# Optimization experiments

Measured on AMD Instinct MI355X. Metric: run time of the kernel, lower is better.

## Reference

```python
import jax, jax.numpy as jnp
import numpy as np

D_MODEL = 512; NHEAD = 8; D_FF = 2048
B = 8; C = 64; P = 128
HALF = D_MODEL // 2        # per-branch embed dim (256)
H_HALF = NHEAD // 2        # per-branch heads (4)
HD = HALF // H_HALF        # per-branch head dim (64)
ROPE_BASE = 10000.0
THETA_SCALE = 2.0 * np.pi
LN_EPS = 1e-5; RMS_EPS = 1e-8


def setup_inputs():
    ks = jax.random.split(jax.random.key(0), 16)
    w = lambda k, s: jax.random.normal(k, s, jnp.float32) * 0.02
    return {
        "src": jax.random.normal(ks[0], (B, C, P, D_MODEL), jnp.float32),
        "coords": jax.random.normal(ks[1], (C, 3), jnp.float32),
        "q_attn": w(ks[2], (D_MODEL,)), "rms_attn": jnp.ones((D_MODEL,), jnp.float32),
        "proj_attn_w": w(ks[3], (D_MODEL, D_MODEL)), "proj_attn_b": jnp.zeros((D_MODEL,), jnp.float32),
        "q_ffn": w(ks[4], (D_MODEL,)), "rms_ffn": jnp.ones((D_MODEL,), jnp.float32),
        "proj_ffn_w": w(ks[5], (D_MODEL, D_MODEL)), "proj_ffn_b": jnp.zeros((D_MODEL,), jnp.float32),
        "ln1_w": jnp.ones((D_MODEL,), jnp.float32), "ln1_b": jnp.zeros((D_MODEL,), jnp.float32),
        "ln2_w": jnp.ones((D_MODEL,), jnp.float32), "ln2_b": jnp.zeros((D_MODEL,), jnp.float32),
        "qkv_s_w": w(ks[6], (3 * HALF, HALF)), "qkv_s_b": jnp.zeros((3 * HALF,), jnp.float32),
        "out_s_w": w(ks[7], (HALF, HALF)), "out_s_b": jnp.zeros((HALF,), jnp.float32),
        "qkv_t_w": w(ks[8], (3 * HALF, HALF)), "qkv_t_b": jnp.zeros((3 * HALF,), jnp.float32),
        "out_t_w": w(ks[9], (HALF, HALF)), "out_t_b": jnp.zeros((HALF,), jnp.float32),
        "w1": w(ks[10], (D_FF, D_MODEL)), "b1": jnp.zeros((D_FF,), jnp.float32),
        "w2": w(ks[11], (D_MODEL, D_FF)), "b2": jnp.zeros((D_MODEL,), jnp.float32),
    }


def _rmsnorm(x, w):
    return x / jnp.sqrt(jnp.mean(x * x, axis=-1, keepdims=True) + RMS_EPS) * w


def _layernorm(x, w, b):
    m = jnp.mean(x, axis=-1, keepdims=True)
    v = jnp.mean((x - m) ** 2, axis=-1, keepdims=True)
    return (x - m) / jnp.sqrt(v + LN_EPS) * w + b


def _attn_residual(src, q, norm_w, proj_w, proj_b):
    # sources = [src] stacked on a leading n-axis (n=1) as in AttentionResidual
    V = src[None]                                  # (n, B, C, P, D)
    K = _rmsnorm(V, norm_w)
    logits = jnp.einsum('d,nbcpd->nbcp', q, K)
    wgt = jax.nn.softmax(logits, axis=0)
    out = jnp.einsum('nbcp,nbcpd->bcpd', wgt, V)
    return out @ proj_w.T + proj_b


def _build_freqs(half, dtype):
    idx = jnp.arange(half, dtype=dtype)
    return 1.0 / ROPE_BASE ** (idx / max(half, 1))


def _coord_rope(coords, half):
    # coords: (L, 3); returns cos, sin of shape (1, 1, L, half)
    axis_ids = jnp.arange(half) % 3
    c = coords - jnp.mean(coords, axis=0, keepdims=True)
    r = jnp.linalg.norm(c, axis=-1)
    c = c / jnp.maximum(jnp.max(r), 1e-6)
    freqs = _build_freqs(half, coords.dtype)
    theta = THETA_SCALE * (c[:, axis_ids] * freqs[None, :])   # (L, half)
    return jnp.cos(theta)[None, None], jnp.sin(theta)[None, None]


def _index_rope(L, half, dtype):
    freqs = _build_freqs(half, dtype)
    pos = jnp.arange(L, dtype=dtype)[:, None]
    theta = pos * freqs[None, :]                               # (L, half)
    return jnp.cos(theta)[None, None], jnp.sin(theta)[None, None]


def _apply_rope(q, k, cos, sin):
    half = q.shape[-1] // 2
    q1, q2 = q[..., :half], q[..., half:]
    k1, k2 = k[..., :half], k[..., half:]
    qr = jnp.concatenate([q1 * cos - q2 * sin, q1 * sin + q2 * cos], axis=-1)
    kr = jnp.concatenate([k1 * cos - k2 * sin, k1 * sin + k2 * cos], axis=-1)
    return qr, kr


def _mha(x, w_qkv, b_qkv, w_o, b_o, H, cos, sin):
    Bx, L, E = x.shape
    Hd = E // H
    qkv = x @ w_qkv.T + b_qkv
    q, k, v = jnp.split(qkv, 3, axis=-1)
    q = q.reshape(Bx, L, H, Hd).transpose(0, 2, 1, 3)   # (B, H, L, Hd)
    k = k.reshape(Bx, L, H, Hd).transpose(0, 2, 1, 3)
    v = v.reshape(Bx, L, H, Hd).transpose(0, 2, 1, 3)
    q, k = _apply_rope(q, k, cos, sin)
    scores = jnp.einsum('bhld,bhmd->bhlm', q, k) * (Hd ** -0.5)
    attn = jax.nn.softmax(scores, axis=-1)
    out = jnp.einsum('bhlm,bhmd->bhld', attn, v)
    out = out.transpose(0, 2, 1, 3).reshape(Bx, L, E)
    return out @ w_o.T + b_o


def reference(src, coords, q_attn, rms_attn, proj_attn_w, proj_attn_b,
              q_ffn, rms_ffn, proj_ffn_w, proj_ffn_b,
              ln1_w, ln1_b, ln2_w, ln2_b,
              qkv_s_w, qkv_s_b, out_s_w, out_s_b,
              qkv_t_w, qkv_t_b, out_t_w, out_t_b,
              w1, b1, w2, b2):
    Bx, Cx, Px, D = src.shape
    half = D // 2
    # --- attention block (pre-norm, attention-residual shortcut) ---
    res1 = _attn_residual(src, q_attn, rms_attn, proj_attn_w, proj_attn_b)
    x = _layernorm(src, ln1_w, ln1_b)
    # spatial branch: attention over channels with coordinate RoPE
    xs = x[..., :half].transpose(0, 2, 1, 3).reshape(Bx * Px, Cx, half)
    cos_s, sin_s = _coord_rope(coords, HD // 2)
    ys = _mha(xs, qkv_s_w, qkv_s_b, out_s_w, out_s_b, H_HALF, cos_s, sin_s)
    ys = ys.reshape(Bx, Px, Cx, half).transpose(0, 2, 1, 3)
    # temporal branch: attention over patches with index RoPE
    xt = x[..., half:].reshape(Bx * Cx, Px, half)
    cos_t, sin_t = _index_rope(Px, HD // 2, src.dtype)
    yt = _mha(xt, qkv_t_w, qkv_t_b, out_t_w, out_t_b, H_HALF, cos_t, sin_t)
    yt = yt.reshape(Bx, Cx, Px, half)
    x = res1 + jnp.concatenate([ys, yt], axis=-1)
    # --- FFN block ---
    res2 = _attn_residual(x, q_ffn, rms_ffn, proj_ffn_w, proj_ffn_b)
    y = _layernorm(x, ln2_w, ln2_b)
    ff = jax.nn.gelu(y @ w1.T + b1, approximate=False) @ w2.T + b2
    return res2 + ff
```

## Files before the change

### kernel.cpp

```cpp
#include <hip/hip_runtime.h>
#include <math.h>
#include <type_traits>

using u16 = unsigned short;
using u32 = unsigned int;

typedef __bf16 bf16x8 __attribute__((ext_vector_type(8)));
typedef float f32x4 __attribute__((ext_vector_type(4)));

__device__ __forceinline__ float lof(u32 u) { u32 x = u << 16; float f; __builtin_memcpy(&f, &x, 4); return f; }
__device__ __forceinline__ float hif(u32 u) { u32 x = u & 0xffff0000u; float f; __builtin_memcpy(&f, &x, 4); return f; }
__device__ __forceinline__ u16 f2bf(float f) {
  u32 u; __builtin_memcpy(&u, &f, 4);
  u32 r = u + 0x7fffu + ((u >> 16) & 1u);
  return (u16)(r >> 16);
}
__device__ __forceinline__ u32 pack2(float a, float b) { return (u32)f2bf(a) | ((u32)f2bf(b) << 16); }
__device__ __forceinline__ float bf2f(u16 s) { u32 x = ((u32)s) << 16; float f; __builtin_memcpy(&f, &x, 4); return f; }
__device__ __forceinline__ float elem(const u32* arr, int j) { u32 u = arr[j >> 1]; return (j & 1) ? hif(u) : lof(u); }

__device__ __forceinline__ void gload_lds16(const u16* g, u16* l) {
  __builtin_amdgcn_global_load_lds((const __attribute__((address_space(1))) void*)g,
                                   (__attribute__((address_space(3))) void*)l, 16, 0, 0);
}

__device__ __forceinline__ float gelu_f(float x) {
  float x3 = x * x * x;
  float u = fmaf(x3, 0.07135481283f, 1.5957691216f * x);
  float e = __expf(u);
  float r = __builtin_amdgcn_rcpf(e + 1.0f);
  return x * e * r;
}

#define NTOK 65536

#define WB_PA   0
#define WB_PF   262144
#define WB_QS   524288
#define WB_QT   720896
#define WB_OS   917504
#define WB_OT   983040
#define WB_W1   1048576
#define WB_W2F  2097152
#define WB_TOT  3407872

#define UC_US 0
#define UC_CS 768
#define UC_UT 1536
#define UC_CT 2304
#define UC_U1 3072
#define UC_C1 5120
#define UC_BC 7168

constexpr size_t O_WB  = 0;
constexpr size_t O_TAB = 6815744;
constexpr size_t O_ST1 = 6864896;
constexpr size_t O_ST2 = 7389184;
constexpr size_t O_UC  = 7913472;
constexpr size_t O_X   = 7944192;
constexpr size_t O_HB  = O_X + (size_t)NTOK * 512 * 2;

__global__ __launch_bounds__(256) void convert_weights_kernel(
    const float* __restrict__ pa, const float* __restrict__ pf,
    const float* __restrict__ qs, const float* __restrict__ qt,
    const float* __restrict__ os_, const float* __restrict__ ot,
    const float* __restrict__ w1, const float* __restrict__ w2,
    const float* __restrict__ ln1w, const float* __restrict__ ln2w,
    u16* __restrict__ dst)
{
  int i = blockIdx.x * 256 + threadIdx.x;
  if (i >= WB_TOT) return;
  float v;
  if (i < 262144)       { v = pa[i]; }
  else if (i < 524288)  { v = pf[i - 262144]; }
  else if (i < 720896)  { int l = i - 524288;  v = qs[l] * ln1w[l & 255]; }
  else if (i < 917504)  { int l = i - 720896;  v = qt[l] * ln1w[256 + (l & 255)]; }
  else if (i < 983040)  { v = os_[i - 917504]; }
  else if (i < 1048576) { v = ot[i - 983040]; }
  else if (i < 2097152) { int l = i - 1048576; v = w1[l] * ln2w[l & 511]; }
  else {
    int l = i - 2097152; int row = l / 2560, col = l - row * 2560;
    v = (col < 2048) ? w2[row * 2048 + col] : pf[row * 512 + (col - 2048)];
  }
  dst[i] = f2bf(v);
}

__global__ __launch_bounds__(256) void ucvec_kernel(
    const float* __restrict__ qs, const float* __restrict__ qt, const float* __restrict__ w1,
    const float* __restrict__ ln1w, const float* __restrict__ ln1b,
    const float* __restrict__ ln2w, const float* __restrict__ ln2b,
    const float* __restrict__ b2, const float* __restrict__ pfb,
    float* __restrict__ uc)
{
  int j = blockIdx.x * 256 + threadIdx.x;
  if (j < 768) {
    float u = 0.f, c = 0.f;
    for (int k = 0; k < 256; k++) { float w = qs[j * 256 + k]; u += ln1w[k] * w; c += ln1b[k] * w; }
    uc[UC_US + j] = u; uc[UC_CS + j] = c;
  } else if (j < 1536) {
    int jj = j - 768; float u = 0.f, c = 0.f;
    for (int k = 0; k < 256; k++) { float w = qt[jj * 256 + k]; u += ln1w[256 + k] * w; c += ln1b[256 + k] * w; }
    uc[UC_UT + jj] = u; uc[UC_CT + jj] = c;
  } else if (j < 3584) {
    int jj = j - 1536; float u = 0.f, c = 0.f;
    for (int k = 0; k < 512; k++) { float w = w1[jj * 512 + k]; u += ln2w[k] * w; c += ln2b[k] * w; }
    uc[UC_U1 + jj] = u; uc[UC_C1 + jj] = c;
  } else if (j < 4096) {
    int jj = j - 3584;
    uc[UC_BC + jj] = b2[jj] + pfb[jj];
  }
}

__global__ __launch_bounds__(256) void rope_tables_kernel(const float* __restrict__ coords, float* __restrict__ tab)
{
  __shared__ float cs[192];
  __shared__ float mean3[3];
  __shared__ float rmax;
  int t = threadIdx.x;
  if (t < 192) cs[t] = coords[t];
  __syncthreads();
  if (t < 3) { float s = 0.f; for (int i = 0; i < 64; i++) s += cs[i * 3 + t]; mean3[t] = s * (1.0f / 64.0f); }
  __syncthreads();
  if (t < 192) cs[t] -= mean3[t % 3];
  __syncthreads();
  if (t == 0) {
    float mx = 0.f;
    for (int i = 0; i < 64; i++) {
      float x = cs[i * 3], y = cs[i * 3 + 1], z = cs[i * 3 + 2];
      mx = fmaxf(mx, sqrtf(x * x + y * y + z * z));
    }
    rmax = fmaxf(mx, 1e-6f);
  }
  __syncthreads();
  float inv = 1.0f / rmax;
  for (int e = t; e < 2048; e += 256) {
    int c = e >> 5, j = e & 31;
    float freq = 1.0f / powf(10000.0f, (float)j * (1.0f / 32.0f));
    float th = 6.283185307179586f * (cs[c * 3 + (j % 3)] * inv) * freq;
    tab[e] = cosf(th); tab[2048 + e] = sinf(th);
  }
  for (int e = t; e < 4096; e += 256) {
    int p = e >> 5, j = e & 31;
    float freq = 1.0f / powf(10000.0f, (float)j * (1.0f / 32.0f));
    float th = (float)p * freq;
    tab[4096 + e] = cosf(th); tab[8192 + e] = sinf(th);
  }
}

__global__ __launch_bounds__(256) void ln_stats_f32_kernel(
    const float* __restrict__ xin, float2* __restrict__ st, u16* __restrict__ srcb)
{
  const int tok = blockIdx.x * 4 + (threadIdx.x >> 6);
  const int lane = threadIdx.x & 63;
  const float* row = xin + (size_t)tok * 512 + lane * 8;
  float4 v0 = ((const float4*)row)[0];
  float4 v1 = ((const float4*)row)[1];
  float v[8] = {v0.x, v0.y, v0.z, v0.w, v1.x, v1.y, v1.z, v1.w};
  float s = 0.f, ss = 0.f;
#pragma unroll
  for (int j = 0; j < 8; j++) { s += v[j]; ss += v[j] * v[j]; }
#pragma unroll
  for (int o = 32; o > 0; o >>= 1) { s += __shfl_xor(s, o); ss += __shfl_xor(ss, o); }
  if (lane == 0) {
    float mean = s * (1.0f / 512.0f);
    float rstd = rsqrtf(ss * (1.0f / 512.0f) - mean * mean + 1e-5f);
    st[tok] = make_float2(mean, rstd);
  }
  if (srcb) {
    uint4 o; u32* op = (u32*)&o;
#pragma unroll
    for (int d = 0; d < 4; d++) op[d] = pack2(v[2 * d], v[2 * d + 1]);
    *(uint4*)(srcb + (size_t)tok * 512 + lane * 8) = o;
  }
}

__global__ __launch_bounds__(256) void ln_stats_bf16_kernel(const u16* __restrict__ xin, float2* __restrict__ st)
{
  const int tok = blockIdx.x * 4 + (threadIdx.x >> 6);
  const int lane = threadIdx.x & 63;
  uint4 u = ((const uint4*)(xin + (size_t)tok * 512))[lane];
  u32 uu[4] = {u.x, u.y, u.z, u.w};
  float s = 0.f, ss = 0.f;
#pragma unroll
  for (int d = 0; d < 4; d++) {
    float a = lof(uu[d]), b = hif(uu[d]);
    s += a + b; ss += a * a + b * b;
  }
#pragma unroll
  for (int o = 32; o > 0; o >>= 1) { s += __shfl_xor(s, o); ss += __shfl_xor(ss, o); }
  if (lane == 0) {
    float mean = s * (1.0f / 512.0f);
    float rstd = rsqrtf(ss * (1.0f / 512.0f) - mean * mean + 1e-5f);
    st[tok] = make_float2(mean, rstd);
  }
}

template<int AMODE, int EMODE, typename OutT>
__global__ __launch_bounds__(512, 2) void gemm256_kernel(
    const u16* __restrict__ A16, int lda,
    const u16* __restrict__ A2, int lda2,
    const u16* __restrict__ Wt, int ldw,
    OutT* __restrict__ C, int ldc,
    const float* __restrict__ bias,
    const float2* __restrict__ stats,
    const float* __restrict__ uvec, const float* __restrict__ cvec,
    int K)
{
  __shared__ u16 As[3][256 * 32];
  __shared__ u16 Bs[3][256 * 32];
  const int t = threadIdx.x;
  const int lane = t & 63, wid = t >> 6;
  const int wm = wid >> 2, wn = wid & 3;
  const int l15 = lane & 15, l4 = lane >> 4;
  const int r0 = t >> 2;
  const int chs = (t & 3) ^ ((t >> 3) & 3);

  const int ntn = gridDim.x;
  const int nwg = ntn * gridDim.y;
  int flat = blockIdx.y * ntn + blockIdx.x;
  int q = nwg >> 3, rmd = nwg & 7, xcd = flat & 7, idx = flat >> 3;
  int wg = (xcd < rmd ? xcd * (q + 1) : rmd * (q + 1) + (xcd - rmd) * q) + idx;
  const int m0 = (wg / ntn) * 256, n0 = (wg % ntn) * 256;

  f32x4 acc[8][4] = {};

  const size_t arow0 = (size_t)(m0 + r0);
  const u16* Wp = Wt + (size_t)(n0 + r0) * ldw + chs * 8;
  const size_t wstep = (size_t)128 * ldw;
  const int nt = K >> 5;

  auto stage = [&](int ti, int buf) {
    const int kk = ti << 5;
    const int cbk = kk + chs * 8;
    const u16* pa; size_t rstep;
    if constexpr (AMODE == 4) {
      if (kk < 2048) { pa = A16 + arow0 * lda + cbk;          rstep = (size_t)128 * lda; }
      else           { pa = A2 + arow0 * lda2 + (cbk - 2048); rstep = (size_t)128 * lda2; }
    } else {
      pa = A16 + arow0 * lda + cbk; rstep = (size_t)128 * lda;
    }
    gload_lds16(pa,         &As[buf][t * 8]);
    gload_lds16(pa + rstep, &As[buf][t * 8 + 4096]);
    gload_lds16(Wp + kk,          &Bs[buf][t * 8]);
    gload_lds16(Wp + wstep + kk,  &Bs[buf][t * 8 + 4096]);
  };

  stage(0, 0);
  stage(1, 1);
  const int pco = (l4 ^ ((l15 >> 1) & 3)) * 8;
  int cb = 0;
  for (int ti = 0; ti < nt; ti++) {
    __builtin_amdgcn_sched_barrier(0);
    if (ti + 1 < nt) { asm volatile("s_waitcnt vmcnt(4)" ::: "memory"); }
    else             { asm volatile("s_waitcnt vmcnt(0)" ::: "memory"); }
    __builtin_amdgcn_sched_barrier(0);
    __builtin_amdgcn_s_barrier();
    __builtin_amdgcn_sched_barrier(0);
    if (ti + 2 < nt) {
      int b2 = cb + 2; if (b2 >= 3) b2 -= 3;
      stage(ti + 2, b2);
    }
    bf16x8 af[8], bfr[4];
#pragma unroll
    for (int i = 0; i < 8; i++)
      af[i] = *(const bf16x8*)(&As[cb][(wm * 128 + i * 16 + l15) * 32 + pco]);
#pragma unroll
    for (int j = 0; j < 4; j++)
      bfr[j] = *(const bf16x8*)(&Bs[cb][(wn * 64 + j * 16 + l15) * 32 + pco]);
    __builtin_amdgcn_s_setprio(1);
#pragma unroll
    for (int i = 0; i < 8; i++)
#pragma unroll
      for (int j = 0; j < 4; j++)
        acc[i][j] = __builtin_amdgcn_mfma_f32_16x16x32_bf16(af[i], bfr[j], acc[i][j], 0, 0, 0);
    __builtin_amdgcn_s_setprio(0);
    __builtin_amdgcn_sched_barrier(0);
    cb = cb == 2 ? 0 : cb + 1;
  }

#pragma unroll
  for (int i = 0; i < 8; i++) {
    const int row = m0 + wm * 128 + i * 16 + l4 * 4;
#pragma unroll
    for (int j = 0; j < 4; j++) {
      const int col = n0 + wn * 64 + j * 16 + l15;
      const float bv = bias[col];
#pragma unroll
      for (int rr = 0; rr < 4; rr++) {
        float v = acc[i][j][rr];
        if constexpr (EMODE >= 3) {
          float2 s = stats[row + rr];
          v = s.y * v - s.x * s.y * uvec[col] + cvec[col] + bv;
          if constexpr (EMODE == 4) v = gelu_f(v);
        } else {
          v += bv;
        }
        const size_t idxc = (size_t)(row + rr) * ldc + col;
        if constexpr (std::is_same<OutT, u16>::value) {
          if constexpr (EMODE == 2) v += bf2f(C[idxc]);
          C[idxc] = f2bf(v);
        } else {
          if constexpr (EMODE == 2) v += C[idxc];
          C[idxc] = v;
        }
      }
    }
  }
}

template<int EMODE, typename OutT>
__global__ __launch_bounds__(256) void gemm_f32a_kernel(
    const float* __restrict__ A32, int lda,
    const u16* __restrict__ Wt, int ldw,
    OutT* __restrict__ C, int ldc,
    const float* __restrict__ bias,
    const float2* __restrict__ stats,
    const float* __restrict__ uvec, const float* __restrict__ cvec,
    int K)
{
  const int t = threadIdx.x;
  const int lane = t & 63, wid = t >> 6;
  const int wm = wid >> 1, wn = wid & 1;
  const int l15 = lane & 15, l4 = lane >> 4;
  const int r0 = t >> 2;
  const int ntn = gridDim.x;
  const int nwg = ntn * gridDim.y;
  int flat = blockIdx.y * ntn + blockIdx.x;
  int q = nwg >> 3, rmd = nwg & 7, xcd = flat & 7, idx = flat >> 3;
  int wg = (xcd < rmd ? xcd * (q + 1) : rmd * (q + 1) + (xcd - rmd) * q) + idx;
  const int m0 = (wg / ntn) * 128, n0 = (wg % ntn) * 128;
  f32x4 acc[4][4] = {};
  const size_t arow0 = (size_t)(m0 + r0);
  const int ch = t & 3;
  const u16* Wp = Wt + (size_t)(n0 + r0) * ldw + ch * 8;
  const size_t wstep = (size_t)64 * ldw;
  __shared__ u16 As[128 * 40];
  __shared__ u16 Bs[128 * 32];
  for (int k0 = 0; k0 < K; k0 += 32) {
    const int cbx = k0 + ch * 8;
    uint4 a0, a1;
    float f0[8], f1[8];
    float4 x0 = *(const float4*)(A32 + arow0 * lda + cbx);
    float4 x1 = *(const float4*)(A32 + arow0 * lda + cbx + 4);
    float4 y0 = *(const float4*)(A32 + (arow0 + 64) * lda + cbx);
    float4 y1 = *(const float4*)(A32 + (arow0 + 64) * lda + cbx + 4);
    f0[0]=x0.x; f0[1]=x0.y; f0[2]=x0.z; f0[3]=x0.w; f0[4]=x1.x; f0[5]=x1.y; f0[6]=x1.z; f0[7]=x1.w;
    f1[0]=y0.x; f1[1]=y0.y; f1[2]=y0.z; f1[3]=y0.w; f1[4]=y1.x; f1[5]=y1.y; f1[6]=y1.z; f1[7]=y1.w;
    u32* p0 = (u32*)&a0; u32* p1 = (u32*)&a1;
#pragma unroll
    for (int d = 0; d < 4; d++) { p0[d] = pack2(f0[2*d], f0[2*d+1]); p1[d] = pack2(f1[2*d], f1[2*d+1]); }
    __syncthreads();
    gload_lds16(Wp + k0, Bs + t * 8);
    gload_lds16(Wp + wstep + k0, Bs + t * 8 + 2048);
    *(uint4*)(As + r0 * 40 + ch * 8) = a0;
    *(uint4*)(As + (r0 + 64) * 40 + ch * 8) = a1;
    __syncthreads();
    bf16x8 af[4], bfr[4];
#pragma unroll
    for (int i = 0; i < 4; i++)
      af[i] = *(const bf16x8*)(As + (wm * 64 + i * 16 + l15) * 40 + l4 * 8);
#pragma unroll
    for (int j = 0; j < 4; j++)
      bfr[j] = *(const bf16x8*)(Bs + (wn * 64 + j * 16 + l15) * 32 + l4 * 8);
#pragma unroll
    for (int i = 0; i < 4; i++)
#pragma unroll
      for (int j = 0; j < 4; j++)
        acc[i][j] = __builtin_amdgcn_mfma_f32_16x16x32_bf16(af[i], bfr[j], acc[i][j], 0, 0, 0);
  }
#pragma unroll
  for (int i = 0; i < 4; i++) {
    const int row = m0 + wm * 64 + i * 16 + l4 * 4;
#pragma unroll
    for (int j = 0; j < 4; j++) {
      const int col = n0 + wn * 64 + j * 16 + l15;
      const float bv = bias[col];
#pragma unroll
      for (int rr = 0; rr < 4; rr++) {
        float v = acc[i][j][rr];
        if constexpr (EMODE >= 3) {
          float2 s = stats[row + rr];
          v = s.y * v - s.x * s.y * uvec[col] + cvec[col] + bv;
        } else {
          v += bv;
        }
        const size_t idxc = (size_t)(row + rr) * ldc + col;
        if constexpr (std::is_same<OutT, u16>::value) C[idxc] = f2bf(v);
        else C[idxc] = v;
      }
    }
  }
}

template<int L>
__global__ __launch_bounds__(256) void attn_mfma_kernel(
    const u16* __restrict__ qkv,
    u16* __restrict__ aout,
    const float* __restrict__ tab)
{
  constexpr int KP = 72;
  constexpr int PP = L + 8;
  constexpr int VP = L + 8;
  constexpr int NI = L / 64;
  constexpr int NJ = L / 16;
  constexpr int NK = L / 32;
  __shared__ u16 Ks[L * KP];
  __shared__ u16 Vt[64 * VP];
  __shared__ u16 Ps[L * PP];

  const int t = threadIdx.x;
  const int lane = t & 63;
  const int w = t >> 6;
  const int l15 = lane & 15, l4 = lane >> 4;
  const int sq = blockIdx.x, h = blockIdx.y;

  long base; int tstride; const float *ct, *st;
  if constexpr (L == 64) { base = (long)(sq >> 7) * 8192 + (sq & 127); tstride = 128; ct = tab;        st = tab + 2048; }
  else                   { base = (long)sq * 128;                      tstride = 1;   ct = tab + 4096; st = tab + 8192; }

  {
    const int tok = t >> 1, hh = t & 1;
    if (tok < L) {
      const size_t rb = (size_t)(base + (long)tok * tstride) * 768 + h * 64;
      u32 ku[32];
#pragma unroll
      for (int i = 0; i < 8; i++) ((uint4*)ku)[i] = ((const uint4*)(qkv + rb + 256))[i];
      const float* cc = ct + tok * 32;
      const float* ss = st + tok * 32;
      u32* kd = (u32*)(Ks + tok * KP + hh * 32);
#pragma unroll
      for (int jj = 0; jj < 16; jj++) {
        float c0 = cc[2*jj], s0 = ss[2*jj], c1 = cc[2*jj+1], s1 = ss[2*jj+1];
        float a0 = elem(ku, 2*jj),     b0 = elem(ku, 2*jj+32);
        float a1 = elem(ku, 2*jj+1),   b1 = elem(ku, 2*jj+33);
        float r0v = hh ? (a0*s0 + b0*c0) : (a0*c0 - b0*s0);
        float r1v = hh ? (a1*s1 + b1*c1) : (a1*c1 - b1*s1);
        kd[jj] = pack2(r0v, r1v);
      }
      u32 vu[16];
#pragma unroll
      for (int i = 0; i < 4; i++) ((uint4*)vu)[i] = ((const uint4*)(qkv + rb + 512 + hh * 32))[i];
#pragma unroll
      for (int j = 0; j < 32; j++)
        Vt[(hh * 32 + j) * VP + tok] = (u16)(vu[j >> 1] >> ((j & 1) * 16));
    }
  }

  bf16x8 aq[NI][2];
#pragma unroll
  for (int i = 0; i < NI; i++) {
    const int row = w * (16 * NI) + i * 16 + l15;
    const u16* qr = qkv + (size_t)(base + (long)row * tstride) * 768 + h * 64;
    uint4 ua = *(const uint4*)(qr + l4 * 8);
    uint4 ub = *(const uint4*)(qr + 32 + l4 * 8);
    u32 au[4] = {ua.x, ua.y, ua.z, ua.w};
    u32 bu[4] = {ub.x, ub.y, ub.z, ub.w};
    const float* cc = ct + row * 32 + l4 * 8;
    const float* ss = st + row * 32 + l4 * 8;
    u32 q0[4], q1[4];
#pragma unroll
    for (int d = 0; d < 4; d++) {
      float a0 = lof(au[d]), a1 = hif(au[d]);
      float b0 = lof(bu[d]), b1 = hif(bu[d]);
      float c0 = cc[2*d], c1 = cc[2*d+1], s0 = ss[2*d], s1 = ss[2*d+1];
      q0[d] = pack2(a0*c0 - b0*s0, a1*c1 - b1*s1);
      q1[d] = pack2(a0*s0 + b0*c0, a1*s1 + b1*c1);
    }
    __builtin_memcpy(&aq[i][0], q0, 16);
    __builtin_memcpy(&aq[i][1], q1, 16);
  }
  __syncthreads();

  f32x4 acc[NI][NJ] = {};
#pragma unroll
  for (int j = 0; j < NJ; j++) {
#pragma unroll
    for (int kk = 0; kk < 2; kk++) {
      bf16x8 bk = *(const bf16x8*)(Ks + (j * 16 + l15) * KP + kk * 32 + l4 * 8);
#pragma unroll
      for (int i = 0; i < NI; i++)
        acc[i][j] = __builtin_amdgcn_mfma_f32_16x16x32_bf16(aq[i][kk], bk, acc[i][j], 0, 0, 0);
    }
  }

  float inv_[NI][4];
#pragma unroll
  for (int i = 0; i < NI; i++) {
#pragma unroll
    for (int rr = 0; rr < 4; rr++) {
      float m = acc[i][0][rr];
#pragma unroll
      for (int j = 1; j < NJ; j++) m = fmaxf(m, acc[i][j][rr]);
      m = fmaxf(m, __shfl_xor(m, 1)); m = fmaxf(m, __shfl_xor(m, 2));
      m = fmaxf(m, __shfl_xor(m, 4)); m = fmaxf(m, __shfl_xor(m, 8));
      m *= 0.125f;
      const int qrow = w * (16 * NI) + i * 16 + l4 * 4 + rr;
      float sm = 0.f;
#pragma unroll
      for (int j = 0; j < NJ; j++) {
        float e = __expf(acc[i][j][rr] * 0.125f - m);
        sm += e;
        Ps[qrow * PP + j * 16 + l15] = f2bf(e);
      }
      sm += __shfl_xor(sm, 1); sm += __shfl_xor(sm, 2);
      sm += __shfl_xor(sm, 4); sm += __shfl_xor(sm, 8);
      inv_[i][rr] = 1.0f / sm;
    }
  }

  f32x4 o[NI][4] = {};
#pragma unroll
  for (int kk = 0; kk < NK; kk++) {
    bf16x8 pa[NI];
#pragma unroll
    for (int i = 0; i < NI; i++)
      pa[i] = *(const bf16x8*)(Ps + (w * (16 * NI) + i * 16 + l15) * PP + kk * 32 + l4 * 8);
#pragma unroll
    for (int jn = 0; jn < 4; jn++) {
      bf16x8 bv = *(const bf16x8*)(Vt + (jn * 16 + l15) * VP + kk * 32 + l4 * 8);
#pragma unroll
      for (int i = 0; i < NI; i++)
        o[i][jn] = __builtin_amdgcn_mfma_f32_16x16x32_bf16(pa[i], bv, o[i][jn], 0, 0, 0);
    }
  }

#pragma unroll
  for (int i = 0; i < NI; i++) {
#pragma unroll
    for (int rr = 0; rr < 4; rr++) {
      const int qrow = w * (16 * NI) + i * 16 + l4 * 4 + rr;
      u16* op = aout + (size_t)(base + (long)qrow * tstride) * 256 + h * 64;
      const float iv = inv_[i][rr];
#pragma unroll
      for (int jn = 0; jn < 4; jn++)
        op[jn * 16 + l15] = f2bf(o[i][jn][rr] * iv);
    }
  }
}

extern "C" void kernel_launch(void* const* d_in, const int* in_sizes, int n_in,
                              void* d_out, int out_size, void* d_ws, size_t ws_size,
                              hipStream_t stream) {
  const float* src         = (const float*)d_in[0];
  const float* coords      = (const float*)d_in[1];
  const float* proj_attn_w = (const float*)d_in[4];
  const float* proj_attn_b = (const float*)d_in[5];
  const float* proj_ffn_w  = (const float*)d_in[8];
  const float* proj_ffn_b  = (const float*)d_in[9];
  const float* ln1_w = (const float*)d_in[10];
  const float* ln1_b = (const float*)d_in[11];
  const float* ln2_w = (const float*)d_in[12];
  const float* ln2_b = (const float*)d_in[13];
  const float* qkv_s_w = (const float*)d_in[14];
  const float* qkv_s_b = (const float*)d_in[15];
  const float* out_s_w = (const float*)d_in[16];
  const float* out_s_b = (const float*)d_in[17];
  const float* qkv_t_w = (const float*)d_in[18];
  const float* qkv_t_b = (const float*)d_in[19];
  const float* out_t_w = (const float*)d_in[20];
  const float* out_t_b = (const float*)d_in[21];
  const float* w1 = (const float*)d_in[22];
  const float* b1 = (const float*)d_in[23];
  const float* w2 = (const float*)d_in[24];
  const float* b2 = (const float*)d_in[25];
  float* out = (float*)d_out;
  char* ws = (char*)d_ws;

  const size_t srcb_bytes = (size_t)NTOK * 512 * 2;
  const int tiers[7] = {65536, 32768, 16384, 8192, 4096, 2048, 512};
  int crows = 0; bool fast = false;
  for (int i = 0; i < 7; i++) {
    size_t need = O_HB + (size_t)tiers[i] * 2048 * 2 + srcb_bytes;
    if (ws_size >= need) { crows = tiers[i]; fast = true; break; }
  }
  if (!crows) {
    for (int i = 0; i < 7; i++)
      if (ws_size >= O_HB + (size_t)tiers[i] * 2048 * 2) { crows = tiers[i]; break; }
  }
  if (!crows) return;
  size_t o_srcb = O_HB + (size_t)crows * 2048 * 2;

  u16*    wb  = (u16*)(ws + O_WB);
  float*  tab = (float*)(ws + O_TAB);
  float2* st1 = (float2*)(ws + O_ST1);
  float2* st2 = (float2*)(ws + O_ST2);
  float*  uc  = (float*)(ws + O_UC);
  u16*    x   = (u16*)(ws + O_X);
  u16*    hb  = (u16*)(ws + O_HB);
  u16*    srcb = fast ? (u16*)(ws + o_srcb) : nullptr;

  u16* qkvb  = (u16*)d_out;
  u16* aoutb = (u16*)((char*)d_out + (size_t)NTOK * 768 * 2);

  convert_weights_kernel<<<(WB_TOT + 255) / 256, 256, 0, stream>>>(
      proj_attn_w, proj_ffn_w, qkv_s_w, qkv_t_w, out_s_w, out_t_w, w1, w2, ln1_w, ln2_w, wb);
  ucvec_kernel<<<16, 256, 0, stream>>>(qkv_s_w, qkv_t_w, w1, ln1_w, ln1_b, ln2_w, ln2_b, b2, proj_ffn_b, uc);
  rope_tables_kernel<<<1, 256, 0, stream>>>(coords, tab);
  ln_stats_f32_kernel<<<NTOK / 4, 256, 0, stream>>>(src, st1, srcb);

  if (fast)
    gemm256_kernel<0, 0, u16><<<dim3(2, 256), 512, 0, stream>>>(srcb, 512, nullptr, 0, wb + WB_PA, 512, x, 512, proj_attn_b, nullptr, nullptr, nullptr, 512);
  else
    gemm_f32a_kernel<0, u16><<<dim3(4, 512), 256, 0, stream>>>(src, 512, wb + WB_PA, 512, x, 512, proj_attn_b, nullptr, nullptr, nullptr, 512);

  if (fast)
    gemm256_kernel<0, 3, u16><<<dim3(3, 256), 512, 0, stream>>>(srcb, 512, nullptr, 0, wb + WB_QS, 256, qkvb, 768, qkv_s_b, st1, uc + UC_US, uc + UC_CS, 256);
  else
    gemm_f32a_kernel<3, u16><<<dim3(6, 512), 256, 0, stream>>>(src, 512, wb + WB_QS, 256, qkvb, 768, qkv_s_b, st1, uc + UC_US, uc + UC_CS, 256);
  attn_mfma_kernel<64><<<dim3(1024, 4), 256, 0, stream>>>(qkvb, aoutb, tab);
  gemm256_kernel<0, 2, u16><<<dim3(1, 256), 512, 0, stream>>>(aoutb, 256, nullptr, 0, wb + WB_OS, 256, x, 512, out_s_b, nullptr, nullptr, nullptr, 256);

  if (fast)
    gemm256_kernel<0, 3, u16><<<dim3(3, 256), 512, 0, stream>>>(srcb + 256, 512, nullptr, 0, wb + WB_QT, 256, qkvb, 768, qkv_t_b, st1, uc + UC_UT, uc + UC_CT, 256);
  else
    gemm_f32a_kernel<3, u16><<<dim3(6, 512), 256, 0, stream>>>(src + 256, 512, wb + WB_QT, 256, qkvb, 768, qkv_t_b, st1, uc + UC_UT, uc + UC_CT, 256);
  attn_mfma_kernel<128><<<dim3(512, 4), 256, 0, stream>>>(qkvb, aoutb, tab);
  gemm256_kernel<0, 2, u16><<<dim3(1, 256), 512, 0, stream>>>(aoutb, 256, nullptr, 0, wb + WB_OT, 256, x + 256, 512, out_t_b, nullptr, nullptr, nullptr, 256);

  ln_stats_bf16_kernel<<<NTOK / 4, 256, 0, stream>>>(x, st2);

  for (int r = 0; r < NTOK; r += crows) {
    gemm256_kernel<0, 4, u16><<<dim3(8, crows / 256), 512, 0, stream>>>(
        x + (size_t)r * 512, 512, nullptr, 0, wb + WB_W1, 512, hb, 2048, b1, st2 + r, uc + UC_U1, uc + UC_C1, 512);
    gemm256_kernel<4, 0, float><<<dim3(2, crows / 256), 512, 0, stream>>>(
        hb, 2048, x + (size_t)r * 512, 512, wb + WB_W2F, 2560, out + (size_t)r * 512, 512, uc + UC_BC, nullptr, nullptr, nullptr, 2560);
  }
}
```

Before: 977.5 us.

## Add 128x128 double-buffered GEMM for small projections and LDS-staged bf16 epilogue

Introduces a 128x128-tile, double-buffered GEMM kernel with XCD-aware block remapping and uses it for the projection, QKV and out-projection GEMMs instead of the 256-tile kernel. The aim is more workgroups to improve occupancy and load balance on these small-K GEMMs. The 256-tile kernel's bf16 epilogue now stages results through LDS and writes 16-byte coalesced rows instead of scattered 2-byte stores. This benefits the large W1 GEMM output, at the cost of extra LDS traffic and a barrier.

```diff
diff --git a/kernel.cpp b/kernel.cpp
--- a/kernel.cpp
+++ b/kernel.cpp
@@ -195,6 +195,109 @@
   }
 }
 
+template<int EMODE, typename OutT>
+__global__ __launch_bounds__(256) void gemm128_kernel(
+    const u16* __restrict__ A16, int lda,
+    const u16* __restrict__ Wt, int ldw,
+    OutT* __restrict__ C, int ldc,
+    const float* __restrict__ bias,
+    const float2* __restrict__ stats,
+    const float* __restrict__ uvec, const float* __restrict__ cvec,
+    int K)
+{
+  const int t = threadIdx.x;
+  const int lane = t & 63, wid = t >> 6;
+  const int wm = wid >> 1, wn = wid & 1;
+  const int l15 = lane & 15, l4 = lane >> 4;
+
+  const int ntn = gridDim.x;
+  const int nwg = ntn * gridDim.y;
+  int flat = blockIdx.y * ntn + blockIdx.x;
+  int q = nwg >> 3, rmd = nwg & 7, xcd = flat & 7, idx = flat >> 3;
+  int wg = (xcd < rmd ? xcd * (q + 1) : rmd * (q + 1) + (xcd - rmd) * q) + idx;
+  const int m0 = (wg / ntn) * 128, n0 = (wg % ntn) * 128;
+
+  f32x4 acc[4][4] = {};
+  const int r0 = t >> 2;
+  const size_t arow0 = (size_t)(m0 + r0);
+
+  __shared__ u16 Asb[2][128 * 32];
+  __shared__ u16 Bsb[2][128 * 32];
+  const int chs = (t & 3) ^ ((t >> 3) & 3);
+  const u16* Wp = Wt + (size_t)(n0 + r0) * ldw + chs * 8;
+  const size_t wstep = (size_t)64 * ldw;
+  const int nt = K / 32;
+  auto stage = [&](int ti, int buf) {
+    const int kk = ti * 32;
+    const u16* pa = A16 + arow0 * lda + kk + chs * 8;
+    const size_t rstep = (size_t)64 * lda;
+    gload_lds16(pa, &Asb[buf][t * 8]);
+    gload_lds16(pa + rstep, &Asb[buf][t * 8 + 2048]);
+    gload_lds16(Wp + kk, &Bsb[buf][t * 8]);
+    gload_lds16(Wp + wstep + kk, &Bsb[buf][t * 8 + 2048]);
+  };
+  stage(0, 0);
+  int cur = 0;
+  const int pco = (l4 ^ ((l15 >> 1) & 3)) * 8;
+  for (int ti = 0; ti < nt; ti++) {
+    if (ti + 1 < nt) {
+      stage(ti + 1, cur ^ 1);
+      __builtin_amdgcn_sched_barrier(0);
+      asm volatile("s_waitcnt vmcnt(4)" ::: "memory");
+    } else {
+      __builtin_amdgcn_sched_barrier(0);
+      asm volatile("s_waitcnt vmcnt(0)" ::: "memory");
+    }
+    __builtin_amdgcn_sched_barrier(0);
+    __builtin_amdgcn_s_barrier();
+    __builtin_amdgcn_sched_barrier(0);
+    bf16x8 af[4], bfr[4];
+#pragma unroll
+    for (int i = 0; i < 4; i++)
+      af[i] = *(const bf16x8*)(&Asb[cur][(wm * 64 + i * 16 + l15) * 32 + pco]);
+#pragma unroll
+    for (int j = 0; j < 4; j++)
+      bfr[j] = *(const bf16x8*)(&Bsb[cur][(wn * 64 + j * 16 + l15) * 32 + pco]);
+#pragma unroll
+    for (int i = 0; i < 4; i++)
+#pragma unroll
+      for (int j = 0; j < 4; j++)
+        acc[i][j] = __builtin_amdgcn_mfma_f32_16x16x32_bf16(af[i], bfr[j], acc[i][j], 0, 0, 0);
+    __builtin_amdgcn_sched_barrier(0);
+    __builtin_amdgcn_s_barrier();
+    __builtin_amdgcn_sched_barrier(0);
+    cur ^= 1;
+  }
+
+#pragma unroll
+  for (int i = 0; i < 4; i++) {
+    const int row = m0 + wm * 64 + i * 16 + l4 * 4;
+#pragma unroll
+    for (int j = 0; j < 4; j++) {
+      const int col = n0 + wn * 64 + j * 16 + l15;
+      const float bv = bias[col];
+#pragma unroll
+      for (int rr = 0; rr < 4; rr++) {
+        float v = acc[i][j][rr];
+        if constexpr (EMODE == 3) {
+          float2 s = stats[row + rr];
+          v = s.y * v - s.x * s.y * uvec[col] + cvec[col] + bv;
+        } else {
+          v += bv;
+        }
+        const size_t idxc = (size_t)(row + rr) * ldc + col;
+        if constexpr (std::is_same<OutT, u16>::value) {
+          if constexpr (EMODE == 2) v += bf2f(C[idxc]);
+          C[idxc] = f2bf(v);
+        } else {
+          if constexpr (EMODE == 2) v += C[idxc];
+          C[idxc] = v;
+        }
+      }
+    }
+  }
+}
+
 template<int AMODE, int EMODE, typename OutT>
 __global__ __launch_bounds__(512, 2) void gemm256_kernel(
     const u16* __restrict__ A16, int lda,
@@ -278,30 +381,58 @@
     cb = cb == 2 ? 0 : cb + 1;
   }
 
-#pragma unroll
-  for (int i = 0; i < 8; i++) {
-    const int row = m0 + wm * 128 + i * 16 + l4 * 4;
-#pragma unroll
-    for (int j = 0; j < 4; j++) {
-      const int col = n0 + wn * 64 + j * 16 + l15;
-      const float bv = bias[col];
-#pragma unroll
-      for (int rr = 0; rr < 4; rr++) {
-        float v = acc[i][j][rr];
-        if constexpr (EMODE >= 3) {
-          float2 s = stats[row + rr];
-          v = s.y * v - s.x * s.y * uvec[col] + cvec[col] + bv;
-          if constexpr (EMODE == 4) v = gelu_f(v);
-        } else {
-          v += bv;
+  auto epi = [&](float v, int row, int col) -> float {
+    const float bv = bias[col];
+    if constexpr (EMODE >= 3) {
+      float2 s = stats[row];
+      v = s.y * v - s.x * s.y * uvec[col] + cvec[col] + bv;
+      if constexpr (EMODE == 4) v = gelu_f(v);
+    } else {
+      v += bv;
+    }
+    return v;
+  };
+
+  if constexpr (std::is_same<OutT, u16>::value) {
+    __syncthreads();
+    u16* sl = &As[0][0] + wid * 3072;
+    const int lr = lane >> 3;
+    const int lcb = (lane & 7) * 8;
+#pragma unroll
+    for (int cc = 0; cc < 4; cc++) {
+#pragma unroll
+      for (int ii = 0; ii < 2; ii++) {
+        const int i = cc * 2 + ii;
+        const int rbase = m0 + wm * 128 + i * 16 + l4 * 4;
+#pragma unroll
+        for (int j = 0; j < 4; j++) {
+          const int col = n0 + wn * 64 + j * 16 + l15;
+#pragma unroll
+          for (int rr = 0; rr < 4; rr++) {
+            float v = epi(acc[i][j][rr], rbase + rr, col);
+            sl[(ii * 16 + l4 * 4 + rr) * 66 + j * 16 + l15] = f2bf(v);
+          }
         }
-        const size_t idxc = (size_t)(row + rr) * ldc + col;
-        if constexpr (std::is_same<OutT, u16>::value) {
-          if constexpr (EMODE == 2) v += bf2f(C[idxc]);
-          C[idxc] = f2bf(v);
-        } else {
-          if constexpr (EMODE == 2) v += C[idxc];
-          C[idxc] = v;
+      }
+#pragma unroll
+      for (int ps = 0; ps < 4; ps++) {
+        const int r = ps * 8 + lr;
+        uint4 d = *(const uint4*)(sl + r * 66 + lcb);
+        const int grow = m0 + wm * 128 + cc * 32 + r;
+        *(uint4*)(C + (size_t)grow * ldc + n0 + wn * 64 + lcb) = d;
+      }
+    }
+  } else {
+#pragma unroll
+    for (int i = 0; i < 8; i++) {
+      const int row = m0 + wm * 128 + i * 16 + l4 * 4;
+#pragma unroll
+      for (int j = 0; j < 4; j++) {
+        const int col = n0 + wn * 64 + j * 16 + l15;
+#pragma unroll
+        for (int rr = 0; rr < 4; rr++) {
+          float v = epi(acc[i][j][rr], row + rr, col);
+          C[(size_t)(row + rr) * ldc + col] = v;
         }
       }
     }
@@ -378,7 +509,7 @@
 #pragma unroll
       for (int rr = 0; rr < 4; rr++) {
         float v = acc[i][j][rr];
-        if constexpr (EMODE >= 3) {
+        if constexpr (EMODE == 3) {
           float2 s = stats[row + rr];
           v = s.y * v - s.x * s.y * uvec[col] + cvec[col] + bv;
         } else {
@@ -599,23 +730,23 @@
   ln_stats_f32_kernel<<<NTOK / 4, 256, 0, stream>>>(src, st1, srcb);
 
   if (fast)
-    gemm256_kernel<0, 0, u16><<<dim3(2, 256), 512, 0, stream>>>(srcb, 512, nullptr, 0, wb + WB_PA, 512, x, 512, proj_attn_b, nullptr, nullptr, nullptr, 512);
+    gemm128_kernel<0, u16><<<dim3(4, 512), 256, 0, stream>>>(srcb, 512, wb + WB_PA, 512, x, 512, proj_attn_b, nullptr, nullptr, nullptr, 512);
   else
     gemm_f32a_kernel<0, u16><<<dim3(4, 512), 256, 0, stream>>>(src, 512, wb + WB_PA, 512, x, 512, proj_attn_b, nullptr, nullptr, nullptr, 512);
 
   if (fast)
-    gemm256_kernel<0, 3, u16><<<dim3(3, 256), 512, 0, stream>>>(srcb, 512, nullptr, 0, wb + WB_QS, 256, qkvb, 768, qkv_s_b, st1, uc + UC_US, uc + UC_CS, 256);
+    gemm128_kernel<3, u16><<<dim3(6, 512), 256, 0, stream>>>(srcb, 512, wb + WB_QS, 256, qkvb, 768, qkv_s_b, st1, uc + UC_US, uc + UC_CS, 256);
   else
     gemm_f32a_kernel<3, u16><<<dim3(6, 512), 256, 0, stream>>>(src, 512, wb + WB_QS, 256, qkvb, 768, qkv_s_b, st1, uc + UC_US, uc + UC_CS, 256);
   attn_mfma_kernel<64><<<dim3(1024, 4), 256, 0, stream>>>(qkvb, aoutb, tab);
-  gemm256_kernel<0, 2, u16><<<dim3(1, 256), 512, 0, stream>>>(aoutb, 256, nullptr, 0, wb + WB_OS, 256, x, 512, out_s_b, nullptr, nullptr, nullptr, 256);
+  gemm128_kernel<2, u16><<<dim3(2, 512), 256, 0, stream>>>(aoutb, 256, wb + WB_OS, 256, x, 512, out_s_b, nullptr, nullptr, nullptr, 256);
 
   if (fast)
-    gemm256_kernel<0, 3, u16><<<dim3(3, 256), 512, 0, stream>>>(srcb + 256, 512, nullptr, 0, wb + WB_QT, 256, qkvb, 768, qkv_t_b, st1, uc + UC_UT, uc + UC_CT, 256);
+    gemm128_kernel<3, u16><<<dim3(6, 512), 256, 0, stream>>>(srcb + 256, 512, wb + WB_QT, 256, qkvb, 768, qkv_t_b, st1, uc + UC_UT, uc + UC_CT, 256);
   else
     gemm_f32a_kernel<3, u16><<<dim3(6, 512), 256, 0, stream>>>(src + 256, 512, wb + WB_QT, 256, qkvb, 768, qkv_t_b, st1, uc + UC_UT, uc + UC_CT, 256);
   attn_mfma_kernel<128><<<dim3(512, 4), 256, 0, stream>>>(qkvb, aoutb, tab);
-  gemm256_kernel<0, 2, u16><<<dim3(1, 256), 512, 0, stream>>>(aoutb, 256, nullptr, 0, wb + WB_OT, 256, x + 256, 512, out_t_b, nullptr, nullptr, nullptr, 256);
+  gemm128_kernel<2, u16><<<dim3(2, 512), 256, 0, stream>>>(aoutb, 256, wb + WB_OT, 256, x + 256, 512, out_t_b, nullptr, nullptr, nullptr, 256);
 
   ln_stats_bf16_kernel<<<NTOK / 4, 256, 0, stream>>>(x, st2);
 
```

After: 968.7 us. About the same (-0.9%).
